# Optimization experiments

Hardware: AMD Instinct MI355X
Metric: run time of the kernel (lower is better)

Reference implementation:

```python
import jax, jax.numpy as jnp
import numpy as np

B, S, H = 1, 2048, 2048
NH = 16
Q_LORA, KV_LORA = 1536, 512
D_NOPE, D_ROPE, D_V = 128, 64, 128
D_QK = D_NOPE + D_ROPE  # 192
EPS = 1e-6
ROPE_BASE = 10000.0


def setup_inputs() -> dict:
    key = jax.random.key(0)
    ks = jax.random.split(key, 8)
    def lin(k, fan_in, fan_out):
        # nn.Linear default init, stored as [in, out] for x @ W
        bound = 1.0 / np.sqrt(fan_in)
        return jax.random.uniform(k, (fan_in, fan_out), jnp.float32, -bound, bound)
    return {
        "hidden_states": jax.random.normal(ks[0], (B, S, H), jnp.float32),
        "Wqa": lin(ks[1], H, Q_LORA),
        "q_a_ln_w": jnp.ones((Q_LORA,), jnp.float32),
        "Wqb": lin(ks[2], Q_LORA, NH * D_QK),
        "Wkva": lin(ks[3], H, KV_LORA + D_ROPE),
        "kv_a_ln_w": jnp.ones((KV_LORA,), jnp.float32),
        "Wkvb": lin(ks[4], KV_LORA, NH * (D_NOPE + D_V)),
        "Wo": lin(ks[5], NH * D_V, H),
    }


def _rmsnorm(x, w):
    xf = x.astype(jnp.float32)
    var = jnp.mean(xf * xf, axis=-1, keepdims=True)
    return w * (xf * jax.lax.rsqrt(var + EPS)).astype(x.dtype)


def _rotate_half(x):
    x1, x2 = jnp.split(x, 2, axis=-1)
    return jnp.concatenate((-x2, x1), axis=-1)


def _rope_tables(seq_len, dtype=jnp.float32):
    inv_freq = 1.0 / (ROPE_BASE ** (jnp.arange(0, D_ROPE, 2, dtype=jnp.float32) / D_ROPE))
    t = jnp.arange(seq_len, dtype=jnp.float32)
    freqs = jnp.outer(t, inv_freq)                      # [S, D_ROPE/2]
    emb = jnp.concatenate((freqs, freqs), axis=-1)      # [S, D_ROPE]
    return jnp.cos(emb).astype(dtype), jnp.sin(emb).astype(dtype)


def reference(hidden_states, Wqa, q_a_ln_w, Wqb, Wkva, kv_a_ln_w, Wkvb, Wo):
    bsz, q_len, _ = hidden_states.shape
    scale = D_QK ** -0.5

    # Q path: LoRA down -> RMSNorm -> up
    q = _rmsnorm(hidden_states @ Wqa, q_a_ln_w) @ Wqb            # [B,S,NH*D_QK]
    q = q.reshape(bsz, q_len, NH, D_QK).transpose(0, 2, 1, 3)    # [B,NH,S,D_QK]
    q_nope, q_pe = q[..., :D_NOPE], q[..., D_NOPE:]

    # KV path: compressed latent + shared rope key
    ckv = hidden_states @ Wkva                                    # [B,S,KV_LORA+D_ROPE]
    compressed_kv, k_pe = ckv[..., :KV_LORA], ckv[..., KV_LORA:]
    k_pe = k_pe.reshape(bsz, q_len, 1, D_ROPE).transpose(0, 2, 1, 3)  # [B,1,S,D_ROPE]
    kv = _rmsnorm(compressed_kv, kv_a_ln_w) @ Wkvb                # [B,S,NH*(D_NOPE+D_V)]
    kv = kv.reshape(bsz, q_len, NH, D_NOPE + D_V).transpose(0, 2, 1, 3)
    k_nope, v = kv[..., :D_NOPE], kv[..., D_NOPE:]                # [B,NH,S,D_NOPE], [B,NH,S,D_V]

    # decoupled RoPE on the rope sub-dims
    cos, sin = _rope_tables(q_len, hidden_states.dtype)
    cos = cos[None, None]  # [1,1,S,D_ROPE] broadcast over batch & heads
    sin = sin[None, None]
    q_pe = q_pe * cos + _rotate_half(q_pe) * sin
    k_pe = k_pe * cos + _rotate_half(k_pe) * sin                  # [B,1,S,D_ROPE]

    query = jnp.concatenate([q_nope, q_pe], axis=-1)              # [B,NH,S,D_QK]
    key = jnp.concatenate([k_nope, jnp.broadcast_to(k_pe, (bsz, NH, q_len, D_ROPE))], axis=-1)

    attn = jnp.einsum('bhqd,bhkd->bhqk', query, key) * scale      # [B,NH,S,S]
    causal = jnp.triu(jnp.ones((q_len, q_len), bool), k=1)
    attn = jnp.where(causal, -jnp.inf, attn)
    attn = jax.nn.softmax(attn.astype(jnp.float32), axis=-1).astype(query.dtype)

    out = jnp.einsum('bhqk,bhkd->bhqd', attn, v)                  # [B,NH,S,D_V]
    out = out.transpose(0, 2, 1, 3).reshape(bsz, q_len, NH * D_V)
    return out @ Wo                                               # [B,S,H]
```

## Files before the change

kernel.cpp:

```cpp
#include <hip/hip_runtime.h>
#include <hip/hip_bf16.h>
#include <math.h>

#define S_LEN 2048
#define H_DIM 2048
#define NH 16
#define Q_LORA 1536
#define KV_LORA 512
#define D_NOPE 128
#define D_ROPE 64
#define D_V 128
#define D_QK 192

typedef unsigned short ushort_t;
typedef __attribute__((ext_vector_type(8))) short short8;
typedef __attribute__((ext_vector_type(4))) float f32x4;

__device__ __forceinline__ ushort_t f2bf(float f) {
    unsigned int u = __float_as_uint(f);
    u = (u + 0x7FFFu + ((u >> 16) & 1u)) >> 16;
    return (ushort_t)u;
}
__device__ __forceinline__ float bf2f(ushort_t u) {
    return __uint_as_float(((unsigned int)u) << 16);
}

__device__ __forceinline__ void storeC(float* p, float v) { *p = v; }
__device__ __forceinline__ void storeC(ushort_t* p, float v) { *p = f2bf(v); }

__device__ __forceinline__ void gload_lds16(const ushort_t* g, ushort_t* l) {
    __builtin_amdgcn_global_load_lds(
        (const __attribute__((address_space(1))) unsigned int*)(const void*)g,
        (__attribute__((address_space(3))) unsigned int*)(void*)l, 16, 0, 0);
}

__device__ __forceinline__ float dpp_max16(float x) {
    x = fmaxf(x, __int_as_float(__builtin_amdgcn_update_dpp(0, __float_as_int(x), 0xB1, 0xF, 0xF, true)));
    x = fmaxf(x, __int_as_float(__builtin_amdgcn_update_dpp(0, __float_as_int(x), 0x4E, 0xF, 0xF, true)));
    x = fmaxf(x, __int_as_float(__builtin_amdgcn_update_dpp(0, __float_as_int(x), 0x124, 0xF, 0xF, true)));
    x = fmaxf(x, __int_as_float(__builtin_amdgcn_update_dpp(0, __float_as_int(x), 0x128, 0xF, 0xF, true)));
    return x;
}
__device__ __forceinline__ float dpp_sum16(float x) {
    x += __int_as_float(__builtin_amdgcn_update_dpp(0, __float_as_int(x), 0xB1, 0xF, 0xF, true));
    x += __int_as_float(__builtin_amdgcn_update_dpp(0, __float_as_int(x), 0x4E, 0xF, 0xF, true));
    x += __int_as_float(__builtin_amdgcn_update_dpp(0, __float_as_int(x), 0x124, 0xF, 0xF, true));
    x += __int_as_float(__builtin_amdgcn_update_dpp(0, __float_as_int(x), 0x128, 0xF, 0xF, true));
    return x;
}

__global__ __launch_bounds__(256) void conv_f32_bf16(
    const float* __restrict__ X, ushort_t* __restrict__ Y, int n)
{
    int base = (blockIdx.x * 256 + threadIdx.x) * 4;
    if (base >= n) return;
    float4 v = *(const float4*)(X + base);
    Y[base + 0] = f2bf(v.x);
    Y[base + 1] = f2bf(v.y);
    Y[base + 2] = f2bf(v.z);
    Y[base + 3] = f2bf(v.w);
}

__global__ __launch_bounds__(256) void convT_kernel(
    const float* __restrict__ W, ushort_t* __restrict__ Wt, int K, int N)
{
    __shared__ float tile[32][33];
    const int k0 = blockIdx.y * 32, n0 = blockIdx.x * 32;
    const int tr = threadIdx.x >> 5, tc = threadIdx.x & 31;
    #pragma unroll
    for (int i = 0; i < 4; ++i) {
        int r = tr + i * 8;
        float v = 0.f;
        if (n0 + tc < N) v = W[(size_t)(k0 + r) * N + n0 + tc];
        tile[r][tc] = v;
    }
    __syncthreads();
    #pragma unroll
    for (int i = 0; i < 4; ++i) {
        int r = tr + i * 8;
        Wt[(size_t)(n0 + r) * K + k0 + tc] = f2bf(tile[tc][r]);
    }
}

__global__ __launch_bounds__(256) void rmsnorm_bf16_kernel(
    const ushort_t* __restrict__ X, int inStride,
    ushort_t* __restrict__ Y, int outStride, int K, const float* __restrict__ w)
{
    __shared__ float red[4];
    const ushort_t* x = X + (size_t)blockIdx.x * inStride;
    ushort_t* y = Y + (size_t)blockIdx.x * outStride;
    float ss = 0.f;
    for (int i = threadIdx.x; i < K; i += 256) { float v = bf2f(x[i]); ss += v * v; }
    #pragma unroll
    for (int off = 32; off > 0; off >>= 1) ss += __shfl_down(ss, off);
    int lane = threadIdx.x & 63, wid = threadIdx.x >> 6;
    if (lane == 0) red[wid] = ss;
    __syncthreads();
    float tot = red[0] + red[1] + red[2] + red[3];
    float rs = rsqrtf(tot / (float)K + 1e-6f);
    for (int i = threadIdx.x; i < K; i += 256)
        y[i] = f2bf(bf2f(x[i]) * rs * w[i]);
}

__global__ void rope_bf16_kernel(
    const ushort_t* __restrict__ src, int srcStride, int srcOff,
    ushort_t* __restrict__ dst, int dstStride, int dstOff,
    int headStride, int nHeads)
{
    int idx = blockIdx.x * 256 + threadIdx.x;
    if (idx >= S_LEN * nHeads * 32) return;
    int i = idx & 31;
    int sh = idx >> 5;
    int hh = sh % nHeads;
    int s = sh / nHeads;
    float inv = powf(10000.0f, -(2.0f * i) / 64.0f);
    float ang = (float)s * inv;
    float c = cosf(ang), sn = sinf(ang);
    const ushort_t* p = src + (size_t)s * srcStride + hh * headStride + srcOff;
    ushort_t* q = dst + (size_t)s * dstStride + hh * headStride + dstOff;
    float x1 = bf2f(p[i]), x2 = bf2f(p[i + 32]);
    q[i]      = f2bf(x1 * c - x2 * sn);
    q[i + 32] = f2bf(x2 * c + x1 * sn);
}

__global__ __launch_bounds__(256) void conv_vT_kernel(
    const ushort_t* __restrict__ kv, ushort_t* __restrict__ v16t)
{
    __shared__ ushort_t tile[32][33];
    const int h = blockIdx.z;
    const int s0 = blockIdx.x * 32, d0 = blockIdx.y * 32;
    const int tr = threadIdx.x >> 5, tc = threadIdx.x & 31;
    #pragma unroll
    for (int i = 0; i < 4; ++i) {
        int r = tr + i * 8;
        tile[r][tc] = kv[(size_t)(s0 + r) * 4096 + h * 256 + D_NOPE + d0 + tc];
    }
    __syncthreads();
    #pragma unroll
    for (int i = 0; i < 4; ++i) {
        int r = tr + i * 8;
        v16t[(size_t)h * D_V * S_LEN + (size_t)(d0 + r) * S_LEN + s0 + tc] = tile[tc][r];
    }
}

template <typename CT>
__global__ __launch_bounds__(256) void mfma_gemm_bt(
    const ushort_t* __restrict__ A, const ushort_t* __restrict__ Bt,
    CT* __restrict__ C, int N, int K)
{
    __shared__ ushort_t Al[64 * 32];
    __shared__ ushort_t Bl[128 * 32];
    const int m0 = blockIdx.y * 64, n0 = blockIdx.x * 128;
    const int tid = threadIdx.x;
    const int lane = tid & 63;
    const int w = tid >> 6;
    const int lm = lane & 15, quad = lane >> 4;
    const int wr = w >> 1, wc = w & 1;

    f32x4 acc[2][4];
    #pragma unroll
    for (int a = 0; a < 2; ++a)
        #pragma unroll
        for (int b = 0; b < 4; ++b) acc[a][b] = (f32x4){0.f, 0.f, 0.f, 0.f};

    const int rrow = tid >> 2;
    const int rcol = (tid & 3) * 8;

    for (int k0 = 0; k0 < K; k0 += 32) {
        __syncthreads();
        gload_lds16(A + (size_t)(m0 + rrow) * K + k0 + rcol, Al + tid * 8);
        #pragma unroll
        for (int i = 0; i < 2; ++i) {
            int row = i * 64 + rrow;
            gload_lds16(Bt + (size_t)(n0 + row) * K + k0 + rcol, Bl + (i * 256 + tid) * 8);
        }
        __syncthreads();

        short8 af[2], bf[4];
        #pragma unroll
        for (int t = 0; t < 2; ++t)
            af[t] = *(const short8*)(Al + (wr * 32 + t * 16 + lm) * 32 + quad * 8);
        #pragma unroll
        for (int t = 0; t < 4; ++t)
            bf[t] = *(const short8*)(Bl + (wc * 64 + t * 16 + lm) * 32 + quad * 8);
        #pragma unroll
        for (int mt = 0; mt < 2; ++mt)
            #pragma unroll
            for (int nt = 0; nt < 4; ++nt)
                acc[mt][nt] = __builtin_amdgcn_mfma_f32_16x16x32_bf16(
                    af[mt], bf[nt], acc[mt][nt], 0, 0, 0);
    }

    #pragma unroll
    for (int mt = 0; mt < 2; ++mt)
        #pragma unroll
        for (int nt = 0; nt < 4; ++nt)
            #pragma unroll
            for (int r = 0; r < 4; ++r) {
                int row = m0 + wr * 32 + mt * 16 + quad * 4 + r;
                int col = n0 + wc * 64 + nt * 16 + lm;
                storeC(&C[(size_t)row * N + col], acc[mt][nt][r]);
            }
}

__device__ __forceinline__ void softmax_step(
    f32x4 s[4], int k0, int qw, int lm, int quad,
    float m_[4], float l_[4], f32x4 O[8], ushort_t* ps)
{
    const float scale = 0.07216878364870322f;
    #pragma unroll
    for (int r = 0; r < 4; ++r) {
        int qrow = qw + quad * 4 + r;
        float a[4];
        #pragma unroll
        for (int st = 0; st < 4; ++st)
            a[st] = (k0 + st * 16 + lm <= qrow) ? s[st][r] * scale : -1e30f;
        float mx = dpp_max16(fmaxf(fmaxf(a[0], a[1]), fmaxf(a[2], a[3])));
        float mn = fmaxf(m_[r], mx);
        float p[4];
        #pragma unroll
        for (int st = 0; st < 4; ++st) p[st] = __expf(a[st] - mn);
        float alpha = __expf(m_[r] - mn);
        float psum = dpp_sum16((p[0] + p[1]) + (p[2] + p[3]));
        l_[r] = l_[r] * alpha + psum;
        m_[r] = mn;
        #pragma unroll
        for (int c = 0; c < 8; ++c) O[c][r] *= alpha;
        #pragma unroll
        for (int st = 0; st < 4; ++st)
            ps[(quad * 4 + r) * 72 + st * 16 + lm] = f2bf(p[st]);
    }
}

__global__ __launch_bounds__(128) void mla_attn_kernel(
    const ushort_t* __restrict__ qb, const ushort_t* __restrict__ kvb,
    const ushort_t* __restrict__ kpe, const ushort_t* __restrict__ v16t,
    ushort_t* __restrict__ aout16)
{
    __shared__ ushort_t Kn[4 * 64 * 32];
    __shared__ ushort_t Kr[2 * 64 * 32];
    __shared__ ushort_t Vt[2 * 128 * 32];
    __shared__ ushort_t Ps[2][16][72];

    const int h = blockIdx.x;
    const int q0 = 32 * (63 - blockIdx.y);
    const int w = threadIdx.x >> 6;
    const int lane = threadIdx.x & 63;
    const int lm = lane & 15, quad = lane >> 4;
    const int qw = q0 + 16 * w;
    ushort_t* myPs = &Ps[w][0][0];

    short8 qf[6];
    #pragma unroll
    for (int f = 0; f < 6; ++f)
        qf[f] = *(const short8*)(qb + (size_t)(qw + lm) * 3072 + h * 192 + f * 32 + quad * 8);

    f32x4 O[8];
    #pragma unroll
    for (int c = 0; c < 8; ++c) O[c] = (f32x4){0.f, 0.f, 0.f, 0.f};
    float m_[4] = {-1e30f, -1e30f, -1e30f, -1e30f};
    float l_[4] = {0.f, 0.f, 0.f, 0.f};

    const int skey = lane >> 2;
    const int ssub = (lane & 3) * 8;

    const int kend = q0 + 32;
    for (int k0 = 0; k0 < kend; k0 += 64) {
        __syncthreads();
        {
            #pragma unroll
            for (int fi = 0; fi < 2; ++fi) {
                int f = 2 * w + fi;
                #pragma unroll
                for (int i = 0; i < 4; ++i)
                    gload_lds16(kvb + (size_t)(k0 + i * 16 + skey) * 4096 + h * 256 + f * 32 + ssub,
                                Kn + f * 2048 + i * 512 + lane * 8);
            }
            #pragma unroll
            for (int i = 0; i < 4; ++i)
                gload_lds16(kpe + (size_t)(k0 + i * 16 + skey) * 64 + w * 32 + ssub,
                            Kr + w * 2048 + i * 512 + lane * 8);
            #pragma unroll
            for (int j = 0; j < 8; ++j)
                gload_lds16(v16t + ((size_t)h * 128 + j * 16 + skey) * S_LEN + k0 + w * 32 + ssub,
                            Vt + w * 4096 + j * 512 + lane * 8);
        }
        __syncthreads();

        if (k0 < qw + 16) {
            f32x4 s[4];
            #pragma unroll
            for (int st = 0; st < 4; ++st) s[st] = (f32x4){0.f, 0.f, 0.f, 0.f};
            #pragma unroll
            for (int f = 0; f < 4; ++f)
                #pragma unroll
                for (int st = 0; st < 4; ++st) {
                    short8 kf = *(const short8*)(Kn + f * 2048 + (st * 16 + lm) * 32 + quad * 8);
                    s[st] = __builtin_amdgcn_mfma_f32_16x16x32_bf16(qf[f], kf, s[st], 0, 0, 0);
                }
            #pragma unroll
            for (int f2 = 0; f2 < 2; ++f2)
                #pragma unroll
                for (int st = 0; st < 4; ++st) {
                    short8 kf = *(const short8*)(Kr + f2 * 2048 + (st * 16 + lm) * 32 + quad * 8);
                    s[st] = __builtin_amdgcn_mfma_f32_16x16x32_bf16(qf[4 + f2], kf, s[st], 0, 0, 0);
                }

            softmax_step(s, k0, qw, lm, quad, m_, l_, O, myPs);

            asm volatile("s_waitcnt lgkmcnt(0)" ::: "memory");
            short8 pf0 = *(const short8*)(myPs + lm * 72 + quad * 8);
            short8 pf1 = *(const short8*)(myPs + lm * 72 + 32 + quad * 8);
            #pragma unroll
            for (int c = 0; c < 8; ++c) {
                short8 vf0 = *(const short8*)(Vt + (c * 16 + lm) * 32 + quad * 8);
                short8 vf1 = *(const short8*)(Vt + 4096 + (c * 16 + lm) * 32 + quad * 8);
                O[c] = __builtin_amdgcn_mfma_f32_16x16x32_bf16(pf0, vf0, O[c], 0, 0, 0);
                O[c] = __builtin_amdgcn_mfma_f32_16x16x32_bf16(pf1, vf1, O[c], 0, 0, 0);
            }
        }
    }
    #pragma unroll
    for (int c = 0; c < 8; ++c)
        #pragma unroll
        for (int r = 0; r < 4; ++r) {
            int qrow = qw + quad * 4 + r;
            aout16[(size_t)qrow * 2048 + h * D_V + c * 16 + lm] = f2bf(O[c][r] / l_[r]);
        }
}

extern "C" void kernel_launch(void* const* d_in, const int* in_sizes, int n_in,
                              void* d_out, int out_size, void* d_ws, size_t ws_size,
                              hipStream_t stream)
{
    (void)in_sizes; (void)n_in; (void)out_size; (void)ws_size;
    const float* hs   = (const float*)d_in[0];
    const float* Wqa  = (const float*)d_in[1];
    const float* qlnw = (const float*)d_in[2];
    const float* Wqb  = (const float*)d_in[3];
    const float* Wkva = (const float*)d_in[4];
    const float* klnw = (const float*)d_in[5];
    const float* Wkvb = (const float*)d_in[6];
    const float* Wo   = (const float*)d_in[7];
    float* out = (float*)d_out;

    ushort_t* p = (ushort_t*)d_ws;
    ushort_t* hs16   = p; p += (size_t)S_LEN * H_DIM;
    ushort_t* WcatT  = p; p += (size_t)2176 * H_DIM;
    ushort_t* WqbT   = p; p += (size_t)3072 * Q_LORA;
    ushort_t* WkvbT  = p; p += (size_t)4096 * KV_LORA;
    ushort_t* WoT    = p; p += (size_t)H_DIM * H_DIM;
    ushort_t* cat16r = p; p += (size_t)S_LEN * 2176;
    ushort_t* qa16   = p; p += (size_t)S_LEN * Q_LORA;
    ushort_t* qbuf16 = p; p += (size_t)S_LEN * 3072;
    ushort_t* ckv16n = p; p += (size_t)S_LEN * KV_LORA;
    ushort_t* kpe16  = p; p += (size_t)S_LEN * D_ROPE;
    ushort_t* kv16   = p; p += (size_t)S_LEN * 4096;
    ushort_t* v16t   = p; p += (size_t)NH * D_V * S_LEN;
    ushort_t* aout16 = p; p += (size_t)S_LEN * 2048;

    conv_f32_bf16<<<(S_LEN * H_DIM / 4 + 255) / 256, 256, 0, stream>>>(hs, hs16, S_LEN * H_DIM);
    convT_kernel<<<dim3(Q_LORA / 32, H_DIM / 32), 256, 0, stream>>>(Wqa, WcatT, H_DIM, Q_LORA);
    convT_kernel<<<dim3(640 / 32, H_DIM / 32), 256, 0, stream>>>(
        Wkva, WcatT + (size_t)Q_LORA * H_DIM, H_DIM, 576);
    convT_kernel<<<dim3(3072 / 32, Q_LORA / 32), 256, 0, stream>>>(Wqb, WqbT, Q_LORA, 3072);
    convT_kernel<<<dim3(4096 / 32, KV_LORA / 32), 256, 0, stream>>>(Wkvb, WkvbT, KV_LORA, 4096);
    convT_kernel<<<dim3(H_DIM / 32, H_DIM / 32), 256, 0, stream>>>(Wo, WoT, H_DIM, H_DIM);

    mfma_gemm_bt<ushort_t><<<dim3(2176 / 128, S_LEN / 64), 256, 0, stream>>>(
        hs16, WcatT, cat16r, 2176, H_DIM);
    rmsnorm_bf16_kernel<<<S_LEN, 256, 0, stream>>>(cat16r, 2176, qa16, Q_LORA, Q_LORA, qlnw);
    mfma_gemm_bt<ushort_t><<<dim3(3072 / 128, S_LEN / 64), 256, 0, stream>>>(
        qa16, WqbT, qbuf16, 3072, Q_LORA);
    rmsnorm_bf16_kernel<<<S_LEN, 256, 0, stream>>>(
        cat16r + Q_LORA, 2176, ckv16n, KV_LORA, KV_LORA, klnw);
    rope_bf16_kernel<<<(S_LEN * NH * 32 + 255) / 256, 256, 0, stream>>>(
        qbuf16, 3072, D_NOPE, qbuf16, 3072, D_NOPE, D_QK, NH);
    rope_bf16_kernel<<<(S_LEN * 32 + 255) / 256, 256, 0, stream>>>(
        cat16r, 2176, Q_LORA + KV_LORA, kpe16, D_ROPE, 0, 0, 1);
    mfma_gemm_bt<ushort_t><<<dim3(4096 / 128, S_LEN / 64), 256, 0, stream>>>(
        ckv16n, WkvbT, kv16, 4096, KV_LORA);
    conv_vT_kernel<<<dim3(S_LEN / 32, D_V / 32, NH), 256, 0, stream>>>(kv16, v16t);
    mla_attn_kernel<<<dim3(NH, 64), 128, 0, stream>>>(qbuf16, kv16, kpe16, v16t, aout16);
    mfma_gemm_bt<float><<<dim3(H_DIM / 128, S_LEN / 64), 256, 0, stream>>>(
        aout16, WoT, out, H_DIM, H_DIM);
}
```

Baseline: 377.0 us.

## Fuse both RMSNorms and k_pe RoPE into one kernel; load V directly to registers

Combines the two RMSNorm launches and the shared k_pe RoPE launch into one kernel, with block ranges dispatching to each task, which removes two launches. In the attention kernel, V^T tiles are no longer staged through LDS; each lane loads its V fragments straight from global memory into registers before the QK MFMAs, cutting LDS traffic and footprint. The cost is uncoalesced-ish global reads of V per wave, duplicated across the two waves, and higher register pressure from sixteen short8 V fragments.

```diff
diff --git a/kernel.cpp b/kernel.cpp
--- a/kernel.cpp
+++ b/kernel.cpp
@@ -82,30 +82,49 @@
     }
 }
 
-__global__ __launch_bounds__(256) void rmsnorm_bf16_kernel(
-    const ushort_t* __restrict__ X, int inStride,
-    ushort_t* __restrict__ Y, int outStride, int K, const float* __restrict__ w)
+__global__ __launch_bounds__(256) void fused_norm_ropek(
+    const ushort_t* __restrict__ cat16r, ushort_t* __restrict__ qa16,
+    ushort_t* __restrict__ ckv16n, ushort_t* __restrict__ kpe16,
+    const float* __restrict__ qlnw, const float* __restrict__ klnw)
 {
     __shared__ float red[4];
-    const ushort_t* x = X + (size_t)blockIdx.x * inStride;
-    ushort_t* y = Y + (size_t)blockIdx.x * outStride;
-    float ss = 0.f;
-    for (int i = threadIdx.x; i < K; i += 256) { float v = bf2f(x[i]); ss += v * v; }
-    #pragma unroll
-    for (int off = 32; off > 0; off >>= 1) ss += __shfl_down(ss, off);
-    int lane = threadIdx.x & 63, wid = threadIdx.x >> 6;
-    if (lane == 0) red[wid] = ss;
-    __syncthreads();
-    float tot = red[0] + red[1] + red[2] + red[3];
-    float rs = rsqrtf(tot / (float)K + 1e-6f);
-    for (int i = threadIdx.x; i < K; i += 256)
-        y[i] = f2bf(bf2f(x[i]) * rs * w[i]);
+    const int b = blockIdx.x;
+    if (b < 4096) {
+        const bool isQ = (b < 2048);
+        const int row = isQ ? b : b - 2048;
+        const int K = isQ ? Q_LORA : KV_LORA;
+        const ushort_t* x = cat16r + (size_t)row * 2176 + (isQ ? 0 : Q_LORA);
+        ushort_t* y = (isQ ? qa16 + (size_t)row * Q_LORA : ckv16n + (size_t)row * KV_LORA);
+        const float* wv = isQ ? qlnw : klnw;
+        float ss = 0.f;
+        for (int i = threadIdx.x; i < K; i += 256) { float v = bf2f(x[i]); ss += v * v; }
+        #pragma unroll
+        for (int off = 32; off > 0; off >>= 1) ss += __shfl_down(ss, off);
+        int lane = threadIdx.x & 63, wid = threadIdx.x >> 6;
+        if (lane == 0) red[wid] = ss;
+        __syncthreads();
+        float tot = red[0] + red[1] + red[2] + red[3];
+        float rs = rsqrtf(tot / (float)K + 1e-6f);
+        for (int i = threadIdx.x; i < K; i += 256)
+            y[i] = f2bf(bf2f(x[i]) * rs * wv[i]);
+    } else {
+        int idx = (b - 4096) * 256 + threadIdx.x;
+        if (idx >= S_LEN * 32) return;
+        int i = idx & 31;
+        int s = idx >> 5;
+        float inv = powf(10000.0f, -(2.0f * i) / 64.0f);
+        float ang = (float)s * inv;
+        float c = cosf(ang), sn = sinf(ang);
+        const ushort_t* p = cat16r + (size_t)s * 2176 + Q_LORA + KV_LORA;
+        ushort_t* q = kpe16 + (size_t)s * D_ROPE;
+        float x1 = bf2f(p[i]), x2 = bf2f(p[i + 32]);
+        q[i]      = f2bf(x1 * c - x2 * sn);
+        q[i + 32] = f2bf(x2 * c + x1 * sn);
+    }
 }
 
 __global__ void rope_bf16_kernel(
-    const ushort_t* __restrict__ src, int srcStride, int srcOff,
-    ushort_t* __restrict__ dst, int dstStride, int dstOff,
-    int headStride, int nHeads)
+    ushort_t* __restrict__ X, int rowStride, int dimOffset, int headStride, int nHeads)
 {
     int idx = blockIdx.x * 256 + threadIdx.x;
     if (idx >= S_LEN * nHeads * 32) return;
@@ -116,11 +135,10 @@
     float inv = powf(10000.0f, -(2.0f * i) / 64.0f);
     float ang = (float)s * inv;
     float c = cosf(ang), sn = sinf(ang);
-    const ushort_t* p = src + (size_t)s * srcStride + hh * headStride + srcOff;
-    ushort_t* q = dst + (size_t)s * dstStride + hh * headStride + dstOff;
+    ushort_t* p = X + (size_t)s * rowStride + hh * headStride + dimOffset;
     float x1 = bf2f(p[i]), x2 = bf2f(p[i + 32]);
-    q[i]      = f2bf(x1 * c - x2 * sn);
-    q[i + 32] = f2bf(x2 * c + x1 * sn);
+    p[i]      = f2bf(x1 * c - x2 * sn);
+    p[i + 32] = f2bf(x2 * c + x1 * sn);
 }
 
 __global__ __launch_bounds__(256) void conv_vT_kernel(
@@ -239,7 +257,6 @@
 {
     __shared__ ushort_t Kn[4 * 64 * 32];
     __shared__ ushort_t Kr[2 * 64 * 32];
-    __shared__ ushort_t Vt[2 * 128 * 32];
     __shared__ ushort_t Ps[2][16][72];
 
     const int h = blockIdx.x;
@@ -249,6 +266,7 @@
     const int lm = lane & 15, quad = lane >> 4;
     const int qw = q0 + 16 * w;
     ushort_t* myPs = &Ps[w][0][0];
+    const ushort_t* vh = v16t + (size_t)h * D_V * S_LEN;
 
     short8 qf[6];
     #pragma unroll
@@ -280,14 +298,17 @@
             for (int i = 0; i < 4; ++i)
                 gload_lds16(kpe + (size_t)(k0 + i * 16 + skey) * 64 + w * 32 + ssub,
                             Kr + w * 2048 + i * 512 + lane * 8);
-            #pragma unroll
-            for (int j = 0; j < 8; ++j)
-                gload_lds16(v16t + ((size_t)h * 128 + j * 16 + skey) * S_LEN + k0 + w * 32 + ssub,
-                            Vt + w * 4096 + j * 512 + lane * 8);
         }
         __syncthreads();
 
         if (k0 < qw + 16) {
+            const ushort_t* vbase = vh + (size_t)lm * S_LEN + k0 + quad * 8;
+            short8 vf0[8], vf1[8];
+            #pragma unroll
+            for (int c = 0; c < 8; ++c) {
+                vf0[c] = *(const short8*)(vbase + (size_t)c * 16 * S_LEN);
+                vf1[c] = *(const short8*)(vbase + (size_t)c * 16 * S_LEN + 32);
+            }
             f32x4 s[4];
             #pragma unroll
             for (int st = 0; st < 4; ++st) s[st] = (f32x4){0.f, 0.f, 0.f, 0.f};
@@ -313,10 +334,8 @@
             short8 pf1 = *(const short8*)(myPs + lm * 72 + 32 + quad * 8);
             #pragma unroll
             for (int c = 0; c < 8; ++c) {
-                short8 vf0 = *(const short8*)(Vt + (c * 16 + lm) * 32 + quad * 8);
-                short8 vf1 = *(const short8*)(Vt + 4096 + (c * 16 + lm) * 32 + quad * 8);
-                O[c] = __builtin_amdgcn_mfma_f32_16x16x32_bf16(pf0, vf0, O[c], 0, 0, 0);
-                O[c] = __builtin_amdgcn_mfma_f32_16x16x32_bf16(pf1, vf1, O[c], 0, 0, 0);
+                O[c] = __builtin_amdgcn_mfma_f32_16x16x32_bf16(pf0, vf0[c], O[c], 0, 0, 0);
+                O[c] = __builtin_amdgcn_mfma_f32_16x16x32_bf16(pf1, vf1[c], O[c], 0, 0, 0);
             }
         }
     }
@@ -369,15 +388,11 @@
 
     mfma_gemm_bt<ushort_t><<<dim3(2176 / 128, S_LEN / 64), 256, 0, stream>>>(
         hs16, WcatT, cat16r, 2176, H_DIM);
-    rmsnorm_bf16_kernel<<<S_LEN, 256, 0, stream>>>(cat16r, 2176, qa16, Q_LORA, Q_LORA, qlnw);
+    fused_norm_ropek<<<4096 + 256, 256, 0, stream>>>(cat16r, qa16, ckv16n, kpe16, qlnw, klnw);
     mfma_gemm_bt<ushort_t><<<dim3(3072 / 128, S_LEN / 64), 256, 0, stream>>>(
         qa16, WqbT, qbuf16, 3072, Q_LORA);
-    rmsnorm_bf16_kernel<<<S_LEN, 256, 0, stream>>>(
-        cat16r + Q_LORA, 2176, ckv16n, KV_LORA, KV_LORA, klnw);
     rope_bf16_kernel<<<(S_LEN * NH * 32 + 255) / 256, 256, 0, stream>>>(
-        qbuf16, 3072, D_NOPE, qbuf16, 3072, D_NOPE, D_QK, NH);
-    rope_bf16_kernel<<<(S_LEN * 32 + 255) / 256, 256, 0, stream>>>(
-        cat16r, 2176, Q_LORA + KV_LORA, kpe16, D_ROPE, 0, 0, 1);
+        qbuf16, 3072, D_NOPE, D_QK, NH);
     mfma_gemm_bt<ushort_t><<<dim3(4096 / 128, S_LEN / 64), 256, 0, stream>>>(
         ckv16n, WkvbT, kv16, 4096, KV_LORA);
     conv_vT_kernel<<<dim3(S_LEN / 32, D_V / 32, NH), 256, 0, stream>>>(kv16, v16t);
```

Result: slower. 394.7 us (+4.7%).
